# Kernel tuning notes

Measured on AMD Instinct MI355X. Metric: run time of the kernel, lower is better.

Reference implementation:

```python
import jax, jax.numpy as jnp
import numpy as np

N_NODES = 500000
IN_CH = 128
HID_CH = 128
NUM_GRAPHS = 1024


def setup_inputs() -> dict:
    key = jax.random.key(0)
    k1, k2, k3, k4, k5, k6 = jax.random.split(key, 6)
    x = jax.random.normal(k1, (N_NODES, IN_CH), dtype=jnp.float32)
    batch = jnp.sort(jax.random.randint(k2, (N_NODES,), 0, NUM_GRAPHS, dtype=jnp.int64))
    # Linear weights stored as [in, out] so forward is x @ W + b
    W1 = jax.random.normal(k3, (IN_CH, HID_CH), dtype=jnp.float32) / np.sqrt(IN_CH)
    b1 = jax.random.normal(k4, (HID_CH,), dtype=jnp.float32) * 0.01
    w2 = jax.random.normal(k5, (HID_CH,), dtype=jnp.float32) / np.sqrt(HID_CH)
    b2 = jax.random.normal(k6, (), dtype=jnp.float32) * 0.01
    return {"x": x, "batch": batch, "W1": W1, "b1": b1, "w2": w2, "b2": b2}


def reference(x, batch, W1, b1, w2, b2):
    # MLP attention scores: [N]
    h = jax.nn.relu(x @ W1 + b1)            # [N, H]
    scores = h @ w2 + b2                     # [N]
    # Segment-wise (per-graph) softmax, numerically stable
    seg_max = jax.ops.segment_max(scores, batch, num_segments=NUM_GRAPHS)
    e = jnp.exp(scores - seg_max[batch])     # [N]
    denom = jax.ops.segment_sum(e, batch, num_segments=NUM_GRAPHS)
    attn = e / denom[batch]                  # [N]
    # Weighted scatter-add pooling: [num_graphs, C]
    weighted = x * attn[:, None]
    return jax.ops.segment_sum(weighted, batch, num_segments=NUM_GRAPHS)
```

## Files before the change

kernel.cpp:

```cpp
#include <hip/hip_runtime.h>
#include <math.h>

#define NN 500000
#define CH 128
#define NG 1024
#define GRID 256
#define TILES ((NN + 127) >> 7)

typedef __attribute__((ext_vector_type(8))) short short8v;
typedef __attribute__((ext_vector_type(4))) float f32x4;

__device__ __forceinline__ void bf16_split(float f, unsigned short& h, unsigned short& l){
  const unsigned u = __float_as_uint(f);
  h = (unsigned short)(u >> 16);
  const float hif = __uint_as_float(u & 0xffff0000u);
  const float lof = f - hif;
  l = (unsigned short)(__float_as_uint(lof) >> 16);
}

__device__ __forceinline__ void gld_lds16(const void* g, void* l){
  __builtin_amdgcn_global_load_lds(
      (__attribute__((address_space(1))) void*)g,
      (__attribute__((address_space(3))) void*)l, 16, 0, 0);
}

__global__ __launch_bounds__(256) void prep_kernel(
    const float* __restrict__ W1, unsigned short* __restrict__ Wg,
    const int* __restrict__ batch, int* __restrict__ start){
  const int t = blockIdx.x * 256 + threadIdx.x;
  if (t < 2048){
    const int n  = t >> 4;
    const int k0 = (t & 15) << 3;
    unsigned short hv[8], lv[8];
    #pragma unroll
    for (int i = 0; i < 8; i++)
      bf16_split(W1[(size_t)(k0 + i) * CH + n], hv[i], lv[i]);
    const int byte = (n * 256 + k0 * 2) ^ ((n & 7) << 4);
    *reinterpret_cast<short8v*>(reinterpret_cast<char*>(Wg) + byte) =
        *reinterpret_cast<short8v*>(hv);
    *reinterpret_cast<short8v*>(reinterpret_cast<char*>(Wg) + 32768 + byte) =
        *reinterpret_cast<short8v*>(lv);
  } else if (t <= 2048 + NG){
    const int g = t - 2048;
    const bool is64 = (batch[NN - 1] == 0);
    if (g == NG){ start[NG] = NN; return; }
    int lo = 0, hi = NN;
    while (lo < hi){
      int mid = (lo + hi) >> 1;
      int v = is64 ? batch[2 * mid] : batch[mid];
      if (v < g) lo = mid + 1; else hi = mid;
    }
    start[g] = lo;
  }
}

__global__ __launch_bounds__(256, 1) void scores_mfma(
    const float* __restrict__ x, const unsigned short* __restrict__ Wg,
    const float* __restrict__ b1, const float* __restrict__ w2,
    const float* __restrict__ b2, float* __restrict__ escore)
{
  __shared__ unsigned short WB[2 * CH * CH];
  __shared__ char XS[4 * 16384];

  const int tid = threadIdx.x;
  const int w   = tid >> 6;
  const int l   = tid & 63;
  const int l15 = l & 15;
  const int g   = l >> 4;
  const int x7  = l15 & 7;

  const int bid = blockIdx.x;
  const int ntb = (TILES - 1 - bid) / GRID + 1;
  const int NP  = ntb * 4;
  const float b2v = b2[0];

  float b1r[8], w2r[8];
  #pragma unroll
  for (int ct = 0; ct < 8; ct++){
    b1r[ct] = b1[ct * 16 + l15];
    w2r[ct] = w2[ct * 16 + l15];
  }

  {
    const short8v* __restrict__ src = reinterpret_cast<const short8v*>(Wg);
    short8v* dst = reinterpret_cast<short8v*>(WB);
    #pragma unroll
    for (int it = 0; it < 16; ++it)
      dst[it * 256 + tid] = src[it * 256 + tid];
  }

  auto stage = [&](int P){
    char* base = XS + (P & 3) * 16384;
    const int u  = bid + (P >> 2) * GRID;
    const int ks = P & 3;
    #pragma unroll
    for (int p = 0; p < 4; ++p){
      const int idx = p * 256 + tid;
      const int R = idx >> 3, c = idx & 7;
      int row = u * 128 + R;
      row = row < NN ? row : NN - 1;
      const char* gsrc = (const char*)x + (size_t)row * 512 + ks * 128 + ((c ^ (R & 7)) << 4);
      gld_lds16(gsrc, base + idx * 16);
    }
  };

  stage(0); stage(1); stage(2);
  __syncthreads();

  for (int ti = 0; ti < ntb; ++ti){
    const int tilebase = (bid + ti * GRID) * 128;

    f32x4 acc[2][8];
    #pragma unroll
    for (int a = 0; a < 2; a++)
      #pragma unroll
      for (int b = 0; b < 8; b++) acc[a][b] = (f32x4)0.f;

    #pragma unroll
    for (int ks = 0; ks < 4; ++ks){
      const int P = ti * 4 + ks;
      asm volatile("s_waitcnt vmcnt(8)" ::: "memory");
      __builtin_amdgcn_s_barrier();
      __builtin_amdgcn_sched_barrier(0);
      if (P + 3 < NP) stage(P + 3);

      const char* sb = XS + ks * 16384;

      short8v Ah[2], Al[2];
      #pragma unroll
      for (int nt = 0; nt < 2; ++nt){
        const char* bp = sb + (w * 32 + nt * 16 + l15) * 128;
        float fv[8];
        *reinterpret_cast<float4*>(fv) =
            *reinterpret_cast<const float4*>(bp + (((2 * g)     ^ x7) << 4));
        *reinterpret_cast<float4*>(fv + 4) =
            *reinterpret_cast<const float4*>(bp + (((2 * g + 1) ^ x7) << 4));
        unsigned short hv[8], lv[8];
        #pragma unroll
        for (int j = 0; j < 8; j++) bf16_split(fv[j], hv[j], lv[j]);
        Ah[nt] = *reinterpret_cast<short8v*>(hv);
        Al[nt] = *reinterpret_cast<short8v*>(lv);
      }

      #pragma unroll
      for (int ct = 0; ct < 8; ++ct){
        const int n = ct * 16 + l15;
        const int byte = (n * 256 + ks * 64 + g * 16) ^ ((n & 7) << 4);
        const short8v Bh = *reinterpret_cast<const short8v*>((const char*)WB + byte);
        const short8v Bl = *reinterpret_cast<const short8v*>((const char*)WB + 32768 + byte);
        #pragma unroll
        for (int nt = 0; nt < 2; ++nt){
          acc[nt][ct] = __builtin_amdgcn_mfma_f32_16x16x32_bf16(Ah[nt], Bh, acc[nt][ct], 0, 0, 0);
          acc[nt][ct] = __builtin_amdgcn_mfma_f32_16x16x32_bf16(Al[nt], Bh, acc[nt][ct], 0, 0, 0);
          acc[nt][ct] = __builtin_amdgcn_mfma_f32_16x16x32_bf16(Ah[nt], Bl, acc[nt][ct], 0, 0, 0);
        }
      }
    }

    float myval = 0.f;
    #pragma unroll
    for (int nt = 0; nt < 2; ++nt){
      #pragma unroll
      for (int r = 0; r < 4; ++r){
        float s = 0.f;
        #pragma unroll
        for (int ct = 0; ct < 8; ++ct){
          float h = fmaxf(acc[nt][ct][r] + b1r[ct], 0.f);
          s = fmaf(h, w2r[ct], s);
        }
        s += __shfl_xor(s, 1); s += __shfl_xor(s, 2);
        s += __shfl_xor(s, 4); s += __shfl_xor(s, 8);
        const float got = __shfl(s, ((l >> 2) & 3) << 4);
        if (((l >> 4) == nt) && ((l & 3) == r)) myval = got;
      }
    }
    if (l < 32){
      const int grow = tilebase + w * 32 + l;
      if (grow < NN) escore[grow] = __expf(myval + b2v);
    }
  }
}

__global__ __launch_bounds__(256) void pool_kernel(
    const float* __restrict__ x, const float* __restrict__ es,
    const int* __restrict__ start, float* __restrict__ out){
  const int g = blockIdx.x;
  const int s0 = start[g], s1 = start[g + 1];
  const int tid = threadIdx.x;
  const int c4 = tid & 31;
  const int rg = tid >> 5;

  float4 a0 = make_float4(0.f, 0.f, 0.f, 0.f);
  float4 a1 = make_float4(0.f, 0.f, 0.f, 0.f);
  float d0 = 0.f, d1 = 0.f;
  int i = s0 + rg;
  for (; i + 8 < s1; i += 16){
    const float e0 = es[i];
    const float e1 = es[i + 8];
    const float4 v0 = reinterpret_cast<const float4*>(&x[(size_t)i * CH])[c4];
    const float4 v1 = reinterpret_cast<const float4*>(&x[(size_t)(i + 8) * CH])[c4];
    a0.x = fmaf(e0, v0.x, a0.x); a0.y = fmaf(e0, v0.y, a0.y);
    a0.z = fmaf(e0, v0.z, a0.z); a0.w = fmaf(e0, v0.w, a0.w);
    d0 += e0;
    a1.x = fmaf(e1, v1.x, a1.x); a1.y = fmaf(e1, v1.y, a1.y);
    a1.z = fmaf(e1, v1.z, a1.z); a1.w = fmaf(e1, v1.w, a1.w);
    d1 += e1;
  }
  if (i < s1){
    const float e0 = es[i];
    const float4 v0 = reinterpret_cast<const float4*>(&x[(size_t)i * CH])[c4];
    a0.x = fmaf(e0, v0.x, a0.x); a0.y = fmaf(e0, v0.y, a0.y);
    a0.z = fmaf(e0, v0.z, a0.z); a0.w = fmaf(e0, v0.w, a0.w);
    d0 += e0;
  }
  a0.x += a1.x; a0.y += a1.y; a0.z += a1.z; a0.w += a1.w;
  d0 += d1;

  __shared__ float4 red[8][32];
  __shared__ float redd[8][32];
  red[rg][c4] = a0;
  redd[rg][c4] = d0;
  __syncthreads();
  if (rg < 4){
    float4 o = red[rg + 4][c4], m = red[rg][c4];
    m.x += o.x; m.y += o.y; m.z += o.z; m.w += o.w;
    red[rg][c4] = m;
    redd[rg][c4] += redd[rg + 4][c4];
  }
  __syncthreads();
  if (rg < 2){
    float4 o = red[rg + 2][c4], m = red[rg][c4];
    m.x += o.x; m.y += o.y; m.z += o.z; m.w += o.w;
    red[rg][c4] = m;
    redd[rg][c4] += redd[rg + 2][c4];
  }
  __syncthreads();
  if (rg == 0){
    float4 b0 = red[0][c4], b1v = red[1][c4];
    const float d = redd[0][c4] + redd[1][c4];
    const float inv = d > 0.f ? 1.f / d : 0.f;
    float4 r;
    r.x = (b0.x + b1v.x) * inv; r.y = (b0.y + b1v.y) * inv;
    r.z = (b0.z + b1v.z) * inv; r.w = (b0.w + b1v.w) * inv;
    reinterpret_cast<float4*>(&out[(size_t)g * CH])[c4] = r;
  }
}

extern "C" void kernel_launch(void* const* d_in, const int* in_sizes, int n_in,
                              void* d_out, int out_size, void* d_ws, size_t ws_size,
                              hipStream_t stream){
  const float* x    = (const float*)d_in[0];
  const int*   batch= (const int*)d_in[1];
  const float* W1   = (const float*)d_in[2];
  const float* b1   = (const float*)d_in[3];
  const float* w2   = (const float*)d_in[4];
  const float* b2   = (const float*)d_in[5];
  float* out = (float*)d_out;

  float* es    = (float*)d_ws;
  int*   start = (int*)((char*)d_ws + (size_t)NN * sizeof(float));
  unsigned short* Wg = (unsigned short*)((char*)d_ws + ((ws_size - 65536) & ~(size_t)255));

  prep_kernel<<<13, 256, 0, stream>>>(W1, Wg, batch, start);
  scores_mfma<<<GRID, 256, 0, stream>>>(x, Wg, b1, w2, b2, es);
  pool_kernel<<<NG, 256, 0, stream>>>(x, es, start, out);
}
```

Baseline: 140.4 us.

## Keep W1 fragments in registers and split output columns across eight waves

The scores kernel now runs 512-thread blocks on a 512-block grid. Each of the eight waves covers 64 rows and 32 output columns, and holds its slice of the bf16 hi/lo W1 fragments in registers instead of reading the full weight matrix from LDS. Staging drops from three k-slices in flight to two, and the per-column partial scores are summed across the four column-waves through a small LDS buffer plus an extra barrier. The aim is to cut LDS traffic and raise occupancy, at the cost of more registers, a cross-wave reduction step and irregular vmcnt waits that could be fragile.

After: 135.8 us. -3.3%, faster.

```diff
diff --git a/kernel.cpp b/kernel.cpp
--- a/kernel.cpp
+++ b/kernel.cpp
@@ -4,7 +4,7 @@
 #define NN 500000
 #define CH 128
 #define NG 1024
-#define GRID 256
+#define GRID_S 512
 #define TILES ((NN + 127) >> 7)
 
 typedef __attribute__((ext_vector_type(8))) short short8v;
@@ -22,6 +22,18 @@
   __builtin_amdgcn_global_load_lds(
       (__attribute__((address_space(1))) void*)g,
       (__attribute__((address_space(3))) void*)l, 16, 0, 0);
+}
+
+__device__ __forceinline__ void cvt8(const float4 f0, const float4 f1,
+                                     short8v& Ah, short8v& Al){
+  float fv[8];
+  *reinterpret_cast<float4*>(fv) = f0;
+  *reinterpret_cast<float4*>(fv + 4) = f1;
+  unsigned short hv[8], lv[8];
+  #pragma unroll
+  for (int j = 0; j < 8; j++) bf16_split(fv[j], hv[j], lv[j]);
+  Ah = *reinterpret_cast<short8v*>(hv);
+  Al = *reinterpret_cast<short8v*>(lv);
 }
 
 __global__ __launch_bounds__(256) void prep_kernel(
@@ -35,11 +47,8 @@
     #pragma unroll
     for (int i = 0; i < 8; i++)
       bf16_split(W1[(size_t)(k0 + i) * CH + n], hv[i], lv[i]);
-    const int byte = (n * 256 + k0 * 2) ^ ((n & 7) << 4);
-    *reinterpret_cast<short8v*>(reinterpret_cast<char*>(Wg) + byte) =
-        *reinterpret_cast<short8v*>(hv);
-    *reinterpret_cast<short8v*>(reinterpret_cast<char*>(Wg) + 32768 + byte) =
-        *reinterpret_cast<short8v*>(lv);
+    *reinterpret_cast<short8v*>(Wg + n * 128 + k0) = *reinterpret_cast<short8v*>(hv);
+    *reinterpret_cast<short8v*>(Wg + 16384 + n * 128 + k0) = *reinterpret_cast<short8v*>(lv);
   } else if (t <= 2048 + NG){
     const int g = t - 2048;
     const bool is64 = (batch[NN - 1] == 0);
@@ -54,129 +63,124 @@
   }
 }
 
-__global__ __launch_bounds__(256, 1) void scores_mfma(
+__global__ __launch_bounds__(512, 4) void scores_mfma(
     const float* __restrict__ x, const unsigned short* __restrict__ Wg,
     const float* __restrict__ b1, const float* __restrict__ w2,
     const float* __restrict__ b2, float* __restrict__ escore)
 {
-  __shared__ unsigned short WB[2 * CH * CH];
-  __shared__ char XS[4 * 16384];
+  __shared__ char  XS[4 * 16384];
+  __shared__ float p4[4][128];
+  __shared__ float b1s[CH], w2s[CH];
 
   const int tid = threadIdx.x;
   const int w   = tid >> 6;
   const int l   = tid & 63;
   const int l15 = l & 15;
   const int g   = l >> 4;
-  const int x7  = l15 & 7;
+  const int rw  = w & 1;
+  const int cw  = w >> 1;
 
   const int bid = blockIdx.x;
-  const int ntb = (TILES - 1 - bid) / GRID + 1;
+  const int ntb = (TILES - 1 - bid) / GRID_S + 1;
   const int NP  = ntb * 4;
   const float b2v = b2[0];
 
-  float b1r[8], w2r[8];
+  if (tid < CH){ b1s[tid] = b1[tid]; w2s[tid] = w2[tid]; }
+
+  short8v Bf[2][4][2];
   #pragma unroll
-  for (int ct = 0; ct < 8; ct++){
-    b1r[ct] = b1[ct * 16 + l15];
-    w2r[ct] = w2[ct * 16 + l15];
-  }
-
-  {
-    const short8v* __restrict__ src = reinterpret_cast<const short8v*>(Wg);
-    short8v* dst = reinterpret_cast<short8v*>(WB);
-    #pragma unroll
-    for (int it = 0; it < 16; ++it)
-      dst[it * 256 + tid] = src[it * 256 + tid];
-  }
-
-  auto stage = [&](int P){
-    char* base = XS + (P & 3) * 16384;
-    const int u  = bid + (P >> 2) * GRID;
-    const int ks = P & 3;
-    #pragma unroll
-    for (int p = 0; p < 4; ++p){
-      const int idx = p * 256 + tid;
-      const int R = idx >> 3, c = idx & 7;
-      int row = u * 128 + R;
-      row = row < NN ? row : NN - 1;
-      const char* gsrc = (const char*)x + (size_t)row * 512 + ks * 128 + ((c ^ (R & 7)) << 4);
-      gld_lds16(gsrc, base + idx * 16);
+  for (int ctk = 0; ctk < 2; ++ctk){
+    const int n = (cw * 2 + ctk) * 16 + l15;
+    #pragma unroll
+    for (int kc = 0; kc < 4; ++kc){
+      Bf[ctk][kc][0] = *reinterpret_cast<const short8v*>(Wg + n * 128 + kc * 32 + g * 8);
+      Bf[ctk][kc][1] = *reinterpret_cast<const short8v*>(Wg + 16384 + n * 128 + kc * 32 + g * 8);
+    }
+  }
+
+  int srcoff[2], dstoff[2];
+  #pragma unroll
+  for (int p = 0; p < 2; ++p){
+    const int idx = p * 512 + tid;
+    const int R = idx >> 3, c = idx & 7;
+    srcoff[p] = R * 512 + ((c ^ (R & 7)) << 4);
+    dstoff[p] = idx * 16;
+  }
+  auto stage = [&](int SL){
+    char* base = XS + (SL & 3) * 16384;
+    const size_t tb = (size_t)(bid + (SL >> 2) * GRID_S) * 65536 + (SL & 3) * 128;
+    #pragma unroll
+    for (int p = 0; p < 2; ++p){
+      size_t so = tb + srcoff[p];
+      if (so >= (size_t)NN * 512) so = (size_t)(NN - 1) * 512;
+      gld_lds16((const char*)x + so, base + dstoff[p]);
     }
   };
 
-  stage(0); stage(1); stage(2);
+  const int abase = (rw * 64 + l15) * 128;
+  const int sw0 = ((2 * g)     ^ (l15 & 7)) << 4;
+  const int sw1 = ((2 * g + 1) ^ (l15 & 7)) << 4;
+
+  stage(0); stage(1);
+  asm volatile("s_waitcnt vmcnt(0) lgkmcnt(0)" ::: "memory");
   __syncthreads();
 
   for (int ti = 0; ti < ntb; ++ti){
-    const int tilebase = (bid + ti * GRID) * 128;
-
-    f32x4 acc[2][8];
-    #pragma unroll
-    for (int a = 0; a < 2; a++)
+    const int tilebase = (bid + ti * GRID_S) * 128;
+
+    f32x4 acc[4][2];
+    #pragma unroll
+    for (int a = 0; a < 4; ++a)
       #pragma unroll
-      for (int b = 0; b < 8; b++) acc[a][b] = (f32x4)0.f;
+      for (int b = 0; b < 2; ++b) acc[a][b] = (f32x4)0.f;
 
     #pragma unroll
     for (int ks = 0; ks < 4; ++ks){
       const int P = ti * 4 + ks;
-      asm volatile("s_waitcnt vmcnt(8)" ::: "memory");
+      if (ti == ntb - 1 && ks == 3)
+        asm volatile("s_waitcnt vmcnt(0)" ::: "memory");
+      else if (ks <= 1 && w < 2 && ti > 0)
+        asm volatile("s_waitcnt vmcnt(3)" ::: "memory");
+      else
+        asm volatile("s_waitcnt vmcnt(2)" ::: "memory");
       __builtin_amdgcn_s_barrier();
-      __builtin_amdgcn_sched_barrier(0);
-      if (P + 3 < NP) stage(P + 3);
+      if (P + 2 < NP) stage(P + 2);
 
       const char* sb = XS + ks * 16384;
-
-      short8v Ah[2], Al[2];
       #pragma unroll
-      for (int nt = 0; nt < 2; ++nt){
-        const char* bp = sb + (w * 32 + nt * 16 + l15) * 128;
-        float fv[8];
-        *reinterpret_cast<float4*>(fv) =
-            *reinterpret_cast<const float4*>(bp + (((2 * g)     ^ x7) << 4));
-        *reinterpret_cast<float4*>(fv + 4) =
-            *reinterpret_cast<const float4*>(bp + (((2 * g + 1) ^ x7) << 4));
-        unsigned short hv[8], lv[8];
+      for (int nt = 0; nt < 4; ++nt){
+        const char* bp = sb + abase + nt * 2048;
+        short8v Ah, Al;
+        cvt8(*reinterpret_cast<const float4*>(bp + sw0),
+             *reinterpret_cast<const float4*>(bp + sw1), Ah, Al);
         #pragma unroll
-        for (int j = 0; j < 8; j++) bf16_split(fv[j], hv[j], lv[j]);
-        Ah[nt] = *reinterpret_cast<short8v*>(hv);
-        Al[nt] = *reinterpret_cast<short8v*>(lv);
-      }
-
-      #pragma unroll
-      for (int ct = 0; ct < 8; ++ct){
-        const int n = ct * 16 + l15;
-        const int byte = (n * 256 + ks * 64 + g * 16) ^ ((n & 7) << 4);
-        const short8v Bh = *reinterpret_cast<const short8v*>((const char*)WB + byte);
-        const short8v Bl = *reinterpret_cast<const short8v*>((const char*)WB + 32768 + byte);
-        #pragma unroll
-        for (int nt = 0; nt < 2; ++nt){
-          acc[nt][ct] = __builtin_amdgcn_mfma_f32_16x16x32_bf16(Ah[nt], Bh, acc[nt][ct], 0, 0, 0);
-          acc[nt][ct] = __builtin_amdgcn_mfma_f32_16x16x32_bf16(Al[nt], Bh, acc[nt][ct], 0, 0, 0);
-          acc[nt][ct] = __builtin_amdgcn_mfma_f32_16x16x32_bf16(Ah[nt], Bl, acc[nt][ct], 0, 0, 0);
+        for (int ctk = 0; ctk < 2; ++ctk){
+          acc[nt][ctk] = __builtin_amdgcn_mfma_f32_16x16x32_bf16(Ah, Bf[ctk][ks][0], acc[nt][ctk], 0, 0, 0);
+          acc[nt][ctk] = __builtin_amdgcn_mfma_f32_16x16x32_bf16(Al, Bf[ctk][ks][0], acc[nt][ctk], 0, 0, 0);
+          acc[nt][ctk] = __builtin_amdgcn_mfma_f32_16x16x32_bf16(Ah, Bf[ctk][ks][1], acc[nt][ctk], 0, 0, 0);
         }
       }
     }
 
-    float myval = 0.f;
-    #pragma unroll
-    for (int nt = 0; nt < 2; ++nt){
+    const float b1v0 = b1s[cw * 32 + l15], b1v1 = b1s[cw * 32 + 16 + l15];
+    const float w2v0 = w2s[cw * 32 + l15], w2v1 = w2s[cw * 32 + 16 + l15];
+    #pragma unroll
+    for (int nt = 0; nt < 4; ++nt){
       #pragma unroll
       for (int r = 0; r < 4; ++r){
-        float s = 0.f;
-        #pragma unroll
-        for (int ct = 0; ct < 8; ++ct){
-          float h = fmaxf(acc[nt][ct][r] + b1r[ct], 0.f);
-          s = fmaf(h, w2r[ct], s);
-        }
+        float s = fmaxf(acc[nt][0][r] + b1v0, 0.f) * w2v0;
+        s = fmaf(fmaxf(acc[nt][1][r] + b1v1, 0.f), w2v1, s);
         s += __shfl_xor(s, 1); s += __shfl_xor(s, 2);
         s += __shfl_xor(s, 4); s += __shfl_xor(s, 8);
-        const float got = __shfl(s, ((l >> 2) & 3) << 4);
-        if (((l >> 4) == nt) && ((l & 3) == r)) myval = got;
+        if (l15 == 0) p4[cw][rw * 64 + nt * 16 + g * 4 + r] = s;
       }
     }
-    if (l < 32){
-      const int grow = tilebase + w * 32 + l;
-      if (grow < NN) escore[grow] = __expf(myval + b2v);
+    asm volatile("s_waitcnt lgkmcnt(0)" ::: "memory");
+    __builtin_amdgcn_s_barrier();
+    if (tid < 128){
+      const float s = p4[0][tid] + p4[1][tid] + p4[2][tid] + p4[3][tid] + b2v;
+      const int grow = tilebase + tid;
+      if (grow < NN) escore[grow] = __expf(s);
     }
   }
 }
@@ -262,6 +266,6 @@
   unsigned short* Wg = (unsigned short*)((char*)d_ws + ((ws_size - 65536) & ~(size_t)255));
 
   prep_kernel<<<13, 256, 0, stream>>>(W1, Wg, batch, start);
-  scores_mfma<<<GRID, 256, 0, stream>>>(x, Wg, b1, w2, b2, es);
+  scores_mfma<<<GRID_S, 512, 0, stream>>>(x, Wg, b1, w2, b2, es);
   pool_kernel<<<NG, 256, 0, stream>>>(x, es, start, out);
 }
```
